# Optimization experiments

Hardware: AMD Instinct MI355X
Metric: run time of the kernel (lower is better)

## Reference

```python
import jax, jax.numpy as jnp
import numpy as np

N, E = 50000, 800000
IN_DIM, HID, HEADS, EDGE_DIM, OUT_DIM = 329, 64, 4, 2, 1
NEG_SLOPE = 0.2


def setup_inputs() -> dict:
    key = jax.random.key(0)
    ks = jax.random.split(key, 20)
    p = lambda k, shp: (jax.random.normal(k, shp, dtype=jnp.float32) * 0.1)
    inp = {
        'x': jax.random.normal(ks[0], (N, IN_DIM), dtype=jnp.float32),
        'edge_attr': jax.random.normal(ks[1], (E, EDGE_DIM), dtype=jnp.float32),
        'edge_index': jax.random.randint(ks[2], (2, E), 0, N, dtype=jnp.int32),
        # conv1: GATConv(329 -> 64, heads=4, edge_dim=2), concat=True
        'W1': p(ks[3], (IN_DIM, HEADS * HID)),
        'att_src1': p(ks[4], (HEADS, HID)),
        'att_dst1': p(ks[5], (HEADS, HID)),
        'We1': p(ks[6], (EDGE_DIM, HEADS * HID)),
        'att_e1': p(ks[7], (HEADS, HID)),
        'b1': jnp.zeros((HEADS * HID,), jnp.float32),
        # conv2: GATConv(256 -> 64, heads=1, edge_dim=2), concat=True
        'W2': p(ks[8], (HEADS * HID, HID)),
        'att_src2': p(ks[9], (1, HID)),
        'att_dst2': p(ks[10], (1, HID)),
        'We2': p(ks[11], (EDGE_DIM, HID)),
        'att_e2': p(ks[12], (1, HID)),
        'b2': jnp.zeros((HID,), jnp.float32),
        # fc head
        'Wf': p(ks[13], (HID, OUT_DIM)),
        'bf': jnp.zeros((OUT_DIM,), jnp.float32),
    }
    return inp


def gat_conv(x, src, dst, ea, W, att_src, att_dst, We, att_e, bias, heads, out_ch):
    n = x.shape[0]
    h = (x @ W).reshape(n, heads, out_ch)                    # [N,H,C]
    a_src = (h * att_src).sum(-1)                            # [N,H]
    a_dst = (h * att_dst).sum(-1)                            # [N,H]
    e = (ea @ We).reshape(-1, heads, out_ch)                 # [Et,H,C]
    a_e = (e * att_e).sum(-1)                                # [Et,H]
    alpha = a_src[src] + a_dst[dst] + a_e                    # [Et,H]
    alpha = jnp.where(alpha > 0, alpha, NEG_SLOPE * alpha)   # leaky_relu
    amax = jax.ops.segment_max(alpha, dst, num_segments=n)
    ex = jnp.exp(alpha - amax[dst])
    denom = jax.ops.segment_sum(ex, dst, num_segments=n)
    attn = ex / (denom[dst] + 1e-16)                         # [Et,H]
    out = jax.ops.segment_sum(attn[..., None] * h[src], dst, num_segments=n)
    return out.reshape(n, heads * out_ch) + bias


def reference(x, edge_attr, edge_index, W1, att_src1, att_dst1, We1, att_e1, b1,
              W2, att_src2, att_dst2, We2, att_e2, b2, Wf, bf):
    n = x.shape[0]
    # add_self_loops with fill_value='mean' for edge_attr (PyG GATConv default)
    loop = jnp.arange(n, dtype=edge_index.dtype)
    src = jnp.concatenate([edge_index[0], loop])
    dst = jnp.concatenate([edge_index[1], loop])
    mean_ea = jnp.mean(edge_attr, axis=0)
    ea = jnp.concatenate([edge_attr, jnp.broadcast_to(mean_ea, (n, edge_attr.shape[1]))])
    h = gat_conv(x, src, dst, ea, W1, att_src1, att_dst1, We1, att_e1, b1, HEADS, HID)
    h = jax.nn.elu(h)
    h = gat_conv(h, src, dst, ea, W2, att_src2, att_dst2, We2, att_e2, b2, 1, HID)
    out = h @ Wf + bf
    return out.squeeze(-1)
```

## Files before the change

### kernel.cpp

```cpp
#include <hip/hip_runtime.h>
#include <hip/hip_bf16.h>
#include <math.h>


#define DEVFN __device__ __forceinline__

typedef __attribute__((ext_vector_type(8))) short short8;
typedef __attribute__((ext_vector_type(4))) float f32x4;

DEVFN float wave_reduce_sum(float v) {
    for (int off = 32; off; off >>= 1) v += __shfl_xor(v, off);
    return v;
}

DEVFN ushort f2bf_rne(float f) {
    unsigned u = __float_as_uint(f);
    unsigned r = (u + 0x7fff + ((u >> 16) & 1)) >> 16;
    return (ushort)r;
}
DEVFN float bf2f(ushort b) { return __uint_as_float(((unsigned)b) << 16); }

__global__ void k_init(int* __restrict__ deg, float* __restrict__ meanbuf, int N) {
    int i = blockIdx.x * blockDim.x + threadIdx.x;
    if (i < N) deg[i] = 0;
    if (i < 2) meanbuf[i] = 0.f;
}

__global__ void k_count_mean(const int* __restrict__ dstrow, const float* __restrict__ ea,
                             int* __restrict__ deg, float* __restrict__ meanbuf, int E, int Et) {
    __shared__ float s0s[4], s1s[4];
    int t = blockIdx.x * blockDim.x + threadIdx.x;
    float s0 = 0.f, s1 = 0.f;
    if (t < Et) {
        int d = (t < E) ? dstrow[t] : (t - E);
        atomicAdd(&deg[d], 1);
        if (t < E) {
            float2 v = reinterpret_cast<const float2*>(ea)[t];
            s0 = v.x; s1 = v.y;
        }
    }
    s0 = wave_reduce_sum(s0);
    s1 = wave_reduce_sum(s1);
    int lane = threadIdx.x & 63, w = threadIdx.x >> 6;
    if (lane == 0) { s0s[w] = s0; s1s[w] = s1; }
    __syncthreads();
    if (threadIdx.x == 0) {
        float a = 0.f, b = 0.f;
        for (int i = 0; i < (int)(blockDim.x >> 6); i++) { a += s0s[i]; b += s1s[i]; }
        atomicAdd(&meanbuf[0], a);
        atomicAdd(&meanbuf[1], b);
    }
}

__global__ void k_scan_block(const int* __restrict__ deg, int* __restrict__ rowptr,
                             int* __restrict__ bsums, int N) {
    __shared__ int sd[1024];
    int i = blockIdx.x * 1024 + threadIdx.x;
    sd[threadIdx.x] = (i < N) ? deg[i] : 0;
    __syncthreads();
    for (int off = 1; off < 1024; off <<= 1) {
        int x = (threadIdx.x >= off) ? sd[threadIdx.x - off] : 0;
        __syncthreads();
        sd[threadIdx.x] += x;
        __syncthreads();
    }
    if (i < N) rowptr[i + 1] = sd[threadIdx.x];
    if (threadIdx.x == 1023) bsums[blockIdx.x] = sd[1023];
}

__global__ void k_scan_bsums(const int* __restrict__ bsums, int* __restrict__ boffs, int nb) {
    if (threadIdx.x == 0 && blockIdx.x == 0) {
        int run = 0;
        for (int b = 0; b < nb; b++) { boffs[b] = run; run += bsums[b]; }
    }
}

__global__ void k_scan_finalize(int* __restrict__ rowptr, const int* __restrict__ boffs,
                                int* __restrict__ cursor, int N) {
    int i = blockIdx.x * blockDim.x + threadIdx.x;
    if (i < N) {
        int val = rowptr[i + 1] + boffs[i >> 10];
        rowptr[i + 1] = val;
        if (i + 1 < N) cursor[i + 1] = val;
    }
    if (i == 0) { rowptr[0] = 0; cursor[0] = 0; }
}

__global__ void k_fill(const int* __restrict__ srcrow, const int* __restrict__ dstrow,
                       int* __restrict__ cursor, int* __restrict__ srcid,
                       float2* __restrict__ ea_csr, const float* __restrict__ ea,
                       const float* __restrict__ meanbuf, float invE, int E, int Et) {
    int t = blockIdx.x * blockDim.x + threadIdx.x;
    if (t >= Et) return;
    int d, s; float2 ev;
    if (t < E) {
        d = dstrow[t]; s = srcrow[t];
        ev = reinterpret_cast<const float2*>(ea)[t];
    } else {
        d = t - E; s = t - E;
        ev = make_float2(meanbuf[0] * invE, meanbuf[1] * invE);
    }
    int pos = atomicAdd(&cursor[d], 1);
    srcid[pos] = s;
    ea_csr[pos] = ev;
}

template <int H>
__global__ void k_collapse(const float* __restrict__ We, const float* __restrict__ att_e,
                           float* __restrict__ M) {
    int t = threadIdx.x;
    int lane = t & 63, w = t >> 6;
    int d = w / H, h = w % H;
    float v = We[(d * H + h) * 64 + lane] * att_e[h * 64 + lane];
    v = wave_reduce_sum(v);
    if (lane == 0) M[d * H + h] = v;
}

__global__ void k_split_wT(const float* __restrict__ W, ushort* __restrict__ hiT,
                           ushort* __restrict__ loT, int K, int Nc, int Kpad) {
    int c = blockIdx.x;
    for (int k = threadIdx.x; k < Kpad; k += blockDim.x) {
        float v = (k < K) ? W[(size_t)k * Nc + c] : 0.f;
        ushort h = f2bf_rne(v);
        ushort l = f2bf_rne(v - bf2f(h));
        hiT[(size_t)c * Kpad + k] = h;
        loT[(size_t)c * Kpad + k] = l;
    }
}

template <int MI, int NI>
__global__ __launch_bounds__(256) void k_gemm_mfma(const float* __restrict__ A,
                                                   const ushort* __restrict__ BhT,
                                                   const ushort* __restrict__ BlT,
                                                   float* __restrict__ C,
                                                   ushort* __restrict__ Cbf,
                                                   int M, int K, int Kpad, int ldc) {
    constexpr int BM = 32 * MI, BN = 32 * NI;
    constexpr int LDA = 40;
    __shared__ __align__(16) ushort Ah[BM * LDA];
    __shared__ __align__(16) ushort Al[BM * LDA];
    __shared__ __align__(16) ushort Bh[BN * LDA];
    __shared__ __align__(16) ushort Bl[BN * LDA];

    int tid = threadIdx.x, lane = tid & 63, wid = tid >> 6;
    int wr = wid >> 1, wc = wid & 1;
    int bm = blockIdx.x * BM, bn = blockIdx.y * BN;

    f32x4 acc[MI][NI];
#pragma unroll
    for (int mi = 0; mi < MI; ++mi)
#pragma unroll
        for (int ni = 0; ni < NI; ++ni) acc[mi][ni] = (f32x4){0.f, 0.f, 0.f, 0.f};

    int steps = Kpad / 32;
    for (int s = 0; s < steps; ++s) {
        int k0 = s * 32;
        __syncthreads();
#pragma unroll
        for (int j = 0; j < BM / 32; ++j) {
            int slot = tid + 256 * j;
            int row = slot >> 3, ch = slot & 7;
            int gr = bm + row, kb = k0 + ch * 4;
            float v[4];
#pragma unroll
            for (int e = 0; e < 4; ++e) {
                int kk = kb + e;
                v[e] = (gr < M && kk < K) ? A[(size_t)gr * K + kk] : 0.f;
            }
            ushort h[4], l[4];
#pragma unroll
            for (int e = 0; e < 4; ++e) {
                h[e] = f2bf_rne(v[e]);
                l[e] = f2bf_rne(v[e] - bf2f(h[e]));
            }
            *reinterpret_cast<ushort4*>(&Ah[row * LDA + ch * 4]) = make_ushort4(h[0], h[1], h[2], h[3]);
            *reinterpret_cast<ushort4*>(&Al[row * LDA + ch * 4]) = make_ushort4(l[0], l[1], l[2], l[3]);
        }
#pragma unroll
        for (int j = 0; j < BN / 64; ++j) {
            int slot = tid + 256 * j;
            int n = slot >> 2, ch = slot & 3;
            size_t goff = (size_t)(bn + n) * Kpad + k0 + ch * 8;
            *reinterpret_cast<float4*>(&Bh[n * LDA + ch * 8]) =
                *reinterpret_cast<const float4*>(&BhT[goff]);
            *reinterpret_cast<float4*>(&Bl[n * LDA + ch * 8]) =
                *reinterpret_cast<const float4*>(&BlT[goff]);
        }
        __syncthreads();
        int kg = (lane >> 4) * 8;
        int am = wr * (MI * 16) + (lane & 15);
        int bc = wc * (NI * 16) + (lane & 15);
        short8 ah[MI], al[MI], bh[NI], bl[NI];
#pragma unroll
        for (int mi = 0; mi < MI; ++mi) {
            ah[mi] = *reinterpret_cast<const short8*>(&Ah[(am + mi * 16) * LDA + kg]);
            al[mi] = *reinterpret_cast<const short8*>(&Al[(am + mi * 16) * LDA + kg]);
        }
#pragma unroll
        for (int ni = 0; ni < NI; ++ni) {
            bh[ni] = *reinterpret_cast<const short8*>(&Bh[(bc + ni * 16) * LDA + kg]);
            bl[ni] = *reinterpret_cast<const short8*>(&Bl[(bc + ni * 16) * LDA + kg]);
        }
#pragma unroll
        for (int mi = 0; mi < MI; ++mi)
#pragma unroll
            for (int ni = 0; ni < NI; ++ni) {
                acc[mi][ni] = __builtin_amdgcn_mfma_f32_16x16x32_bf16(ah[mi], bh[ni], acc[mi][ni], 0, 0, 0);
                acc[mi][ni] = __builtin_amdgcn_mfma_f32_16x16x32_bf16(ah[mi], bl[ni], acc[mi][ni], 0, 0, 0);
                acc[mi][ni] = __builtin_amdgcn_mfma_f32_16x16x32_bf16(al[mi], bh[ni], acc[mi][ni], 0, 0, 0);
            }
    }
#pragma unroll
    for (int mi = 0; mi < MI; ++mi) {
        int row0 = bm + wr * (MI * 16) + mi * 16 + ((lane >> 4) << 2);
#pragma unroll
        for (int ni = 0; ni < NI; ++ni) {
            int col = bn + wc * (NI * 16) + ni * 16 + (lane & 15);
            f32x4 v = acc[mi][ni];
#pragma unroll
            for (int r = 0; r < 4; ++r)
                if (row0 + r < M) {
                    C[(size_t)(row0 + r) * ldc + col] = v[r];
                    Cbf[(size_t)(row0 + r) * ldc + col] = f2bf_rne(v[r]);
                }
        }
    }
}

template <int H>
__global__ void k_node_attn(const float* __restrict__ h, const float* __restrict__ att_src,
                            const float* __restrict__ att_dst, float* __restrict__ asrc,
                            float* __restrict__ adst, int N) {
    constexpr int HC = H * 64;
    constexpr int NPB = 256 / HC;
    int local = threadIdx.x % HC;
    int n = blockIdx.x * NPB + threadIdx.x / HC;
    if (n >= N) return;
    float v = h[(size_t)n * HC + local];
    float s = v * att_src[local];
    float d = v * att_dst[local];
    for (int off = 32; off; off >>= 1) { s += __shfl_xor(s, off); d += __shfl_xor(d, off); }
    if ((local & 63) == 0) {
        int hh = local >> 6;
        asrc[n * H + hh] = s;
        adst[n * H + hh] = d;
    }
}

template <int H>
__global__ void k_attn(const int* __restrict__ rowptr, const int* __restrict__ srcid,
                       const float2* __restrict__ ea_csr, const float* __restrict__ asrc,
                       const float* __restrict__ adst, const float* __restrict__ M,
                       float* __restrict__ attn, float* __restrict__ dinv, int N) {
    int lane = threadIdx.x & 63;
    int n = blockIdx.x * 4 + (threadIdx.x >> 6);
    if (n >= N) return;
    int start = rowptr[n];
    int items = (rowptr[n + 1] - start) * H;
    int h = lane % H;
    float ad = adst[n * H + h];
    float m0 = M[h], m1 = M[H + h];

    float mx = -1e30f;
    for (int i = lane; i < items; i += 64) {
        int p = start + i / H;
        int s = srcid[p];
        float2 ev = ea_csr[p];
        float al = asrc[s * H + h] + ad + ev.x * m0 + ev.y * m1;
        al = (al > 0.f) ? al : 0.2f * al;
        attn[(size_t)start * H + i] = al;
        mx = fmaxf(mx, al);
    }
    for (int off = H; off < 64; off <<= 1) mx = fmaxf(mx, __shfl_xor(mx, off));

    float ss = 0.f;
    for (int i = lane; i < items; i += 64) {
        float ex = expf(attn[(size_t)start * H + i] - mx);
        attn[(size_t)start * H + i] = ex;
        ss += ex;
    }
    for (int off = H; off < 64; off <<= 1) ss += __shfl_xor(ss, off);
    if (lane < H) dinv[n * H + h] = 1.f / (ss + 1e-16f);
}

template <int H, bool ELU>
__global__ void k_aggregate_bf(const int* __restrict__ rowptr, const int* __restrict__ srcid,
                               const float* __restrict__ attn, const float* __restrict__ dinv,
                               const ushort* __restrict__ hbf, const float* __restrict__ bias,
                               float* __restrict__ out, int N) {
    constexpr int HC = H * 64;
    constexpr int LPN = HC / 8;
    constexpr int NPB = 256 / LPN;
    int li = threadIdx.x % LPN;
    int n = blockIdx.x * NPB + threadIdx.x / LPN;
    if (n >= N) return;
    int hh = li >> 3;
    const short8* h8 = reinterpret_cast<const short8*>(hbf);
    int start = rowptr[n], end = rowptr[n + 1];
    float acc[8];
#pragma unroll
    for (int j = 0; j < 8; ++j) acc[j] = 0.f;
    int p = start;
    for (; p + 3 < end; p += 4) {
        int s0 = srcid[p], s1 = srcid[p + 1], s2 = srcid[p + 2], s3 = srcid[p + 3];
        float w0 = attn[p * H + hh], w1 = attn[(p + 1) * H + hh];
        float w2 = attn[(p + 2) * H + hh], w3 = attn[(p + 3) * H + hh];
        short8 v0 = h8[(size_t)s0 * LPN + li];
        short8 v1 = h8[(size_t)s1 * LPN + li];
        short8 v2 = h8[(size_t)s2 * LPN + li];
        short8 v3 = h8[(size_t)s3 * LPN + li];
#pragma unroll
        for (int j = 0; j < 8; ++j)
            acc[j] += w0 * bf2f((ushort)v0[j]) + w1 * bf2f((ushort)v1[j]) +
                      w2 * bf2f((ushort)v2[j]) + w3 * bf2f((ushort)v3[j]);
    }
    for (; p < end; ++p) {
        int s = srcid[p];
        float w = attn[p * H + hh];
        short8 v = h8[(size_t)s * LPN + li];
#pragma unroll
        for (int j = 0; j < 8; ++j) acc[j] += w * bf2f((ushort)v[j]);
    }
    float inv = dinv[n * H + hh];
    const float4* b4 = reinterpret_cast<const float4*>(bias);
    float4 ba = b4[li * 2], bb = b4[li * 2 + 1];
    float bv[8] = {ba.x, ba.y, ba.z, ba.w, bb.x, bb.y, bb.z, bb.w};
    float4 o0, o1;
    float* ov = &o0.x;
#pragma unroll
    for (int j = 0; j < 8; ++j) {
        float r = acc[j] * inv + bv[j];
        if (ELU) r = (r > 0.f) ? r : expm1f(r);
        ((j < 4) ? (&o0.x) : (&o1.x))[j & 3] = r;
    }
    (void)ov;
    float4* out4 = reinterpret_cast<float4*>(out);
    out4[(size_t)n * (HC / 4) + li * 2]     = o0;
    out4[(size_t)n * (HC / 4) + li * 2 + 1] = o1;
}

__global__ void k_fc(const float* __restrict__ h, const float* __restrict__ Wf,
                     const float* __restrict__ bf, float* __restrict__ out, int N) {
    int lane = threadIdx.x & 63;
    int n = blockIdx.x * 4 + (threadIdx.x >> 6);
    if (n >= N) return;
    float v = h[(size_t)n * 64 + lane] * Wf[lane];
    v = wave_reduce_sum(v);
    if (lane == 0) out[n] = v + bf[0];
}

extern "C" void kernel_launch(void* const* d_in, const int* in_sizes, int n_in,
                              void* d_out, int out_size, void* d_ws, size_t ws_size,
                              hipStream_t stream) {
    const float* x        = (const float*)d_in[0];
    const float* ea       = (const float*)d_in[1];
    const int*   ei       = (const int*)d_in[2];
    const float* W1       = (const float*)d_in[3];
    const float* att_src1 = (const float*)d_in[4];
    const float* att_dst1 = (const float*)d_in[5];
    const float* We1      = (const float*)d_in[6];
    const float* att_e1   = (const float*)d_in[7];
    const float* b1       = (const float*)d_in[8];
    const float* W2       = (const float*)d_in[9];
    const float* att_src2 = (const float*)d_in[10];
    const float* att_dst2 = (const float*)d_in[11];
    const float* We2      = (const float*)d_in[12];
    const float* att_e2   = (const float*)d_in[13];
    const float* b2       = (const float*)d_in[14];
    const float* Wf       = (const float*)d_in[15];
    const float* bf       = (const float*)d_in[16];

    const int IN_DIM = 329;
    const int K1PAD = 352;
    int N  = in_sizes[0] / IN_DIM;
    int E  = in_sizes[1] / 2;
    int Et = E + N;
    const int* srcrow = ei;
    const int* dstrow = ei + E;

    char* p = (char*)d_ws;
    size_t used = 0;
    auto alloc = [&](size_t bytes) -> void* {
        void* r = p;
        size_t pad = (bytes + 255) & ~(size_t)255;
        p += pad; used += pad;
        return r;
    };
    float*  h1     = (float*)alloc((size_t)N * 256 * 4);
    float*  agg1   = (float*)alloc((size_t)N * 256 * 4);
    ushort* h1bf   = (ushort*)alloc((size_t)N * 256 * 2);
    ushort* h2bf   = (ushort*)alloc((size_t)N * 64 * 2);
    float*  asrc   = (float*)alloc((size_t)N * 4 * 4);
    float*  adst   = (float*)alloc((size_t)N * 4 * 4);
    float*  dinv   = (float*)alloc((size_t)N * 4 * 4);
    float*  attn   = (float*)alloc((size_t)Et * 4 * 4);
    float2* ea_csr = (float2*)alloc((size_t)Et * 8);
    int*    srcid  = (int*)alloc((size_t)Et * 4);
    ushort* w1hT   = (ushort*)alloc((size_t)256 * K1PAD * 2);
    ushort* w1lT   = (ushort*)alloc((size_t)256 * K1PAD * 2);
    ushort* w2hT   = (ushort*)alloc((size_t)64 * 256 * 2);
    ushort* w2lT   = (ushort*)alloc((size_t)64 * 256 * 2);
    float*  M1     = (float*)alloc(256);
    float*  M2     = (float*)alloc(256);
    float*  meanbuf= (float*)alloc(256);
    int*    rowptr = (int*)alloc((size_t)(N + 1) * 4);
    int*    deg    = (int*)alloc((size_t)N * 4);
    int*    bsums  = (int*)alloc(1024);
    int*    boffs  = (int*)alloc(1024);
    if (used > ws_size) return;

    int gN  = (N + 255) / 256;
    int gEt = (Et + 255) / 256;
    int nb  = (N + 1023) / 1024;
    int gM  = (N + 127) / 128;
    float invE = 1.f / (float)E;

    k_init<<<gN, 256, 0, stream>>>(deg, meanbuf, N);
    k_count_mean<<<gEt, 256, 0, stream>>>(dstrow, ea, deg, meanbuf, E, Et);
    k_scan_block<<<nb, 1024, 0, stream>>>(deg, rowptr, bsums, N);
    k_scan_bsums<<<1, 64, 0, stream>>>(bsums, boffs, nb);
    k_scan_finalize<<<gN, 256, 0, stream>>>(rowptr, boffs, deg , N);
    k_fill<<<gEt, 256, 0, stream>>>(srcrow, dstrow, deg, srcid, ea_csr, ea, meanbuf, invE, E, Et);

    k_collapse<4><<<1, 512, 0, stream>>>(We1, att_e1, M1);
    k_collapse<1><<<1, 128, 0, stream>>>(We2, att_e2, M2);
    k_split_wT<<<256, 384, 0, stream>>>(W1, w1hT, w1lT, IN_DIM, 256, K1PAD);
    k_split_wT<<<64, 256, 0, stream>>>(W2, w2hT, w2lT, 256, 64, 256);

    k_gemm_mfma<4, 4><<<dim3(gM, 2), 256, 0, stream>>>(x, w1hT, w1lT, h1, h1bf, N, IN_DIM, K1PAD, 256);
    k_node_attn<4><<<N, 256, 0, stream>>>(h1, att_src1, att_dst1, asrc, adst, N);
    k_attn<4><<<(N + 3) / 4, 256, 0, stream>>>(rowptr, srcid, ea_csr, asrc, adst, M1, attn, dinv, N);
    k_aggregate_bf<4, true><<<(N + 7) / 8, 256, 0, stream>>>(rowptr, srcid, attn, dinv,
                                                             h1bf, b1, agg1, N);

    k_gemm_mfma<4, 2><<<dim3(gM, 1), 256, 0, stream>>>(agg1, w2hT, w2lT, h1 , h2bf, N, 256, 256, 64);
    k_node_attn<1><<<(N + 3) / 4, 256, 0, stream>>>(h1, att_src2, att_dst2, asrc, adst, N);
    k_attn<1><<<(N + 3) / 4, 256, 0, stream>>>(rowptr, srcid, ea_csr, asrc, adst, M2, attn, dinv, N);
    k_aggregate_bf<1, false><<<(N + 31) / 32, 256, 0, stream>>>(rowptr, srcid, attn, dinv,
                                                                h2bf, b2, agg1 , N);

    k_fc<<<(N + 3) / 4, 256, 0, stream>>>(agg1, Wf, bf, (float*)d_out, N);
}
```

Before: 551.6 us.

## Precompute per-edge CSR rank, split mean reduction, and fuse final aggregate with FC head

The degree-count pass now records each edge's atomic rank, so the fill pass computes its CSR position as rowptr[d]+rank with no second atomic pass over the cursor array. The edge-attribute mean moves into a separate grid-stride kernel instead of per-block atomics on every count block. The layer-2 aggregation is fused with the final linear head, which removes the N×64 intermediate write and read and one kernel launch. In exchange it adds an Et-sized rank buffer plus the writes and reads of it, and one extra launch for the mean kernel.

```diff
diff --git a/kernel.cpp b/kernel.cpp
--- a/kernel.cpp
+++ b/kernel.cpp
@@ -26,18 +26,20 @@
     if (i < 2) meanbuf[i] = 0.f;
 }
 
-__global__ void k_count_mean(const int* __restrict__ dstrow, const float* __restrict__ ea,
-                             int* __restrict__ deg, float* __restrict__ meanbuf, int E, int Et) {
+__global__ void k_count(const int* __restrict__ dstrow, int* __restrict__ deg,
+                        int* __restrict__ rank, int E, int Et) {
+    int t = blockIdx.x * blockDim.x + threadIdx.x;
+    if (t >= Et) return;
+    int d = (t < E) ? dstrow[t] : (t - E);
+    rank[t] = atomicAdd(&deg[d], 1);
+}
+
+__global__ void k_mean(const float* __restrict__ ea, float* __restrict__ meanbuf, int E) {
     __shared__ float s0s[4], s1s[4];
-    int t = blockIdx.x * blockDim.x + threadIdx.x;
     float s0 = 0.f, s1 = 0.f;
-    if (t < Et) {
-        int d = (t < E) ? dstrow[t] : (t - E);
-        atomicAdd(&deg[d], 1);
-        if (t < E) {
-            float2 v = reinterpret_cast<const float2*>(ea)[t];
-            s0 = v.x; s1 = v.y;
-        }
+    for (int i = blockIdx.x * blockDim.x + threadIdx.x; i < E; i += gridDim.x * blockDim.x) {
+        float2 v = reinterpret_cast<const float2*>(ea)[i];
+        s0 += v.x; s1 += v.y;
     }
     s0 = wave_reduce_sum(s0);
     s1 = wave_reduce_sum(s1);
@@ -75,21 +77,17 @@
     }
 }
 
-__global__ void k_scan_finalize(int* __restrict__ rowptr, const int* __restrict__ boffs,
-                                int* __restrict__ cursor, int N) {
+__global__ void k_scan_finalize(int* __restrict__ rowptr, const int* __restrict__ boffs, int N) {
     int i = blockIdx.x * blockDim.x + threadIdx.x;
-    if (i < N) {
-        int val = rowptr[i + 1] + boffs[i >> 10];
-        rowptr[i + 1] = val;
-        if (i + 1 < N) cursor[i + 1] = val;
-    }
-    if (i == 0) { rowptr[0] = 0; cursor[0] = 0; }
+    if (i < N) rowptr[i + 1] += boffs[i >> 10];
+    if (i == 0) rowptr[0] = 0;
 }
 
 __global__ void k_fill(const int* __restrict__ srcrow, const int* __restrict__ dstrow,
-                       int* __restrict__ cursor, int* __restrict__ srcid,
-                       float2* __restrict__ ea_csr, const float* __restrict__ ea,
-                       const float* __restrict__ meanbuf, float invE, int E, int Et) {
+                       const int* __restrict__ rowptr, const int* __restrict__ rank,
+                       int* __restrict__ srcid, float2* __restrict__ ea_csr,
+                       const float* __restrict__ ea, const float* __restrict__ meanbuf,
+                       float invE, int E, int Et) {
     int t = blockIdx.x * blockDim.x + threadIdx.x;
     if (t >= Et) return;
     int d, s; float2 ev;
@@ -100,7 +98,7 @@
         d = t - E; s = t - E;
         ev = make_float2(meanbuf[0] * invE, meanbuf[1] * invE);
     }
-    int pos = atomicAdd(&cursor[d], 1);
+    int pos = rowptr[d] + rank[t];
     srcid[pos] = s;
     ea_csr[pos] = ev;
 }
@@ -326,27 +324,65 @@
     float4 ba = b4[li * 2], bb = b4[li * 2 + 1];
     float bv[8] = {ba.x, ba.y, ba.z, ba.w, bb.x, bb.y, bb.z, bb.w};
     float4 o0, o1;
-    float* ov = &o0.x;
 #pragma unroll
     for (int j = 0; j < 8; ++j) {
         float r = acc[j] * inv + bv[j];
         if (ELU) r = (r > 0.f) ? r : expm1f(r);
         ((j < 4) ? (&o0.x) : (&o1.x))[j & 3] = r;
     }
-    (void)ov;
     float4* out4 = reinterpret_cast<float4*>(out);
     out4[(size_t)n * (HC / 4) + li * 2]     = o0;
     out4[(size_t)n * (HC / 4) + li * 2 + 1] = o1;
 }
 
-__global__ void k_fc(const float* __restrict__ h, const float* __restrict__ Wf,
-                     const float* __restrict__ bf, float* __restrict__ out, int N) {
-    int lane = threadIdx.x & 63;
-    int n = blockIdx.x * 4 + (threadIdx.x >> 6);
+__global__ void k_aggregate_fc(const int* __restrict__ rowptr, const int* __restrict__ srcid,
+                               const float* __restrict__ attn, const float* __restrict__ dinv,
+                               const ushort* __restrict__ hbf, const float* __restrict__ bias,
+                               const float* __restrict__ Wf, const float* __restrict__ bf,
+                               float* __restrict__ out, int N) {
+    constexpr int LPN = 8;
+    int li = threadIdx.x % LPN;
+    int n = blockIdx.x * 32 + threadIdx.x / LPN;
     if (n >= N) return;
-    float v = h[(size_t)n * 64 + lane] * Wf[lane];
-    v = wave_reduce_sum(v);
-    if (lane == 0) out[n] = v + bf[0];
+    const short8* h8 = reinterpret_cast<const short8*>(hbf);
+    int start = rowptr[n], end = rowptr[n + 1];
+    float acc[8];
+#pragma unroll
+    for (int j = 0; j < 8; ++j) acc[j] = 0.f;
+    int p = start;
+    for (; p + 3 < end; p += 4) {
+        int s0 = srcid[p], s1 = srcid[p + 1], s2 = srcid[p + 2], s3 = srcid[p + 3];
+        float w0 = attn[p], w1 = attn[p + 1], w2 = attn[p + 2], w3 = attn[p + 3];
+        short8 v0 = h8[(size_t)s0 * LPN + li];
+        short8 v1 = h8[(size_t)s1 * LPN + li];
+        short8 v2 = h8[(size_t)s2 * LPN + li];
+        short8 v3 = h8[(size_t)s3 * LPN + li];
+#pragma unroll
+        for (int j = 0; j < 8; ++j)
+            acc[j] += w0 * bf2f((ushort)v0[j]) + w1 * bf2f((ushort)v1[j]) +
+                      w2 * bf2f((ushort)v2[j]) + w3 * bf2f((ushort)v3[j]);
+    }
+    for (; p < end; ++p) {
+        int s = srcid[p];
+        float w = attn[p];
+        short8 v = h8[(size_t)s * LPN + li];
+#pragma unroll
+        for (int j = 0; j < 8; ++j) acc[j] += w * bf2f((ushort)v[j]);
+    }
+    float inv = dinv[n];
+    const float4* b4 = reinterpret_cast<const float4*>(bias);
+    const float4* w4 = reinterpret_cast<const float4*>(Wf);
+    float4 ba = b4[li * 2], bb = b4[li * 2 + 1];
+    float4 wa = w4[li * 2], wb = w4[li * 2 + 1];
+    float bv[8] = {ba.x, ba.y, ba.z, ba.w, bb.x, bb.y, bb.z, bb.w};
+    float wv[8] = {wa.x, wa.y, wa.z, wa.w, wb.x, wb.y, wb.z, wb.w};
+    float partial = 0.f;
+#pragma unroll
+    for (int j = 0; j < 8; ++j) partial += (acc[j] * inv + bv[j]) * wv[j];
+    partial += __shfl_xor(partial, 1);
+    partial += __shfl_xor(partial, 2);
+    partial += __shfl_xor(partial, 4);
+    if (li == 0) out[n] = partial + bf[0];
 }
 
 extern "C" void kernel_launch(void* const* d_in, const int* in_sizes, int n_in,
@@ -396,6 +432,7 @@
     float*  attn   = (float*)alloc((size_t)Et * 4 * 4);
     float2* ea_csr = (float2*)alloc((size_t)Et * 8);
     int*    srcid  = (int*)alloc((size_t)Et * 4);
+    int*    rank   = (int*)alloc((size_t)Et * 4);
     ushort* w1hT   = (ushort*)alloc((size_t)256 * K1PAD * 2);
     ushort* w1lT   = (ushort*)alloc((size_t)256 * K1PAD * 2);
     ushort* w2hT   = (ushort*)alloc((size_t)64 * 256 * 2);
@@ -416,11 +453,13 @@
     float invE = 1.f / (float)E;
 
     k_init<<<gN, 256, 0, stream>>>(deg, meanbuf, N);
-    k_count_mean<<<gEt, 256, 0, stream>>>(dstrow, ea, deg, meanbuf, E, Et);
+    k_count<<<gEt, 256, 0, stream>>>(dstrow, deg, rank, E, Et);
+    k_mean<<<256, 256, 0, stream>>>(ea, meanbuf, E);
     k_scan_block<<<nb, 1024, 0, stream>>>(deg, rowptr, bsums, N);
     k_scan_bsums<<<1, 64, 0, stream>>>(bsums, boffs, nb);
-    k_scan_finalize<<<gN, 256, 0, stream>>>(rowptr, boffs, deg , N);
-    k_fill<<<gEt, 256, 0, stream>>>(srcrow, dstrow, deg, srcid, ea_csr, ea, meanbuf, invE, E, Et);
+    k_scan_finalize<<<gN, 256, 0, stream>>>(rowptr, boffs, N);
+    k_fill<<<gEt, 256, 0, stream>>>(srcrow, dstrow, rowptr, rank, srcid, ea_csr, ea,
+                                    meanbuf, invE, E, Et);
 
     k_collapse<4><<<1, 512, 0, stream>>>(We1, att_e1, M1);
     k_collapse<1><<<1, 128, 0, stream>>>(We2, att_e2, M2);
@@ -436,8 +475,6 @@
     k_gemm_mfma<4, 2><<<dim3(gM, 1), 256, 0, stream>>>(agg1, w2hT, w2lT, h1 , h2bf, N, 256, 256, 64);
     k_node_attn<1><<<(N + 3) / 4, 256, 0, stream>>>(h1, att_src2, att_dst2, asrc, adst, N);
     k_attn<1><<<(N + 3) / 4, 256, 0, stream>>>(rowptr, srcid, ea_csr, asrc, adst, M2, attn, dinv, N);
-    k_aggregate_bf<1, false><<<(N + 31) / 32, 256, 0, stream>>>(rowptr, srcid, attn, dinv,
-                                                                h2bf, b2, agg1 , N);
-
-    k_fc<<<(N + 3) / 4, 256, 0, stream>>>(agg1, Wf, bf, (float*)d_out, N);
-}
+    k_aggregate_fc<<<(N + 31) / 32, 256, 0, stream>>>(rowptr, srcid, attn, dinv,
+                                                      h2bf, b2, Wf, bf, (float*)d_out, N);
+}
```

New measurement: 483.2 us. 1.14x faster.
